# Kernel tuning notes

Hardware: AMD Instinct MI355X
Metric: run time of the kernel (lower is better)

Reference implementation:

```python
import jax, jax.numpy as jnp
import numpy as np

NUM_HEADS = 16
HEAD_DIM = 128
WINDOW = 512
ROPE_BASE = 10000.0


def _rope_cos_sin(seq_len):
    inv_freq = 1.0 / (ROPE_BASE ** (jnp.arange(0, HEAD_DIM, 2, dtype=jnp.float32) / HEAD_DIM))
    freqs = jnp.arange(seq_len, dtype=jnp.float32)[:, None] * inv_freq[None, :]  # (s, d/2)
    return jnp.cos(freqs), jnp.sin(freqs)


def _apply_rotary(x, cos, sin):
    # x: (b, h, s, d); cos/sin: (s, d/2). Interleaved pairs as in the torch impl.
    x1, x2 = x[..., ::2], x[..., 1::2]
    c = cos[None, None]
    s = sin[None, None]
    r1 = x1 * c - x2 * s
    r2 = x1 * s + x2 * c
    return jnp.stack([r1, r2], axis=-1).reshape(x.shape)


def setup_inputs() -> dict:
    key = jax.random.key(0)
    ks = jax.random.split(key, 5)
    dim = NUM_HEADS * HEAD_DIM
    x = jax.random.normal(ks[0], (1, 4096, dim), dtype=jnp.float32)
    std = 0.02
    Wq = jax.random.normal(ks[1], (dim, dim), dtype=jnp.float32) * std
    Wk = jax.random.normal(ks[2], (dim, dim), dtype=jnp.float32) * std
    Wv = jax.random.normal(ks[3], (dim, dim), dtype=jnp.float32) * std
    Wo = jax.random.normal(ks[4], (dim, dim), dtype=jnp.float32) * std
    return {"x": x, "Wq": Wq, "Wk": Wk, "Wv": Wv, "Wo": Wo}


def reference(x, Wq, Wk, Wv, Wo):
    b, s, dim = x.shape
    scale = HEAD_DIM ** -0.5

    def split_heads(t):
        return t.reshape(b, s, NUM_HEADS, HEAD_DIM).transpose(0, 2, 1, 3)  # b h s d

    q = split_heads(x @ Wq.T)
    k = split_heads(x @ Wk.T)
    v = split_heads(x @ Wv.T)

    cos, sin = _rope_cos_sin(s)
    q = _apply_rotary(q, cos, sin)
    k = _apply_rotary(k, cos, sin)

    scores = jnp.einsum('bhqd,bhkd->bhqk', q, k) * scale  # (b, h, s, s)
    pos = jnp.arange(s)
    i, j = pos[:, None], pos[None, :]
    mask = (j <= i) & (i - j < WINDOW)  # sliding-window causal
    scores = jnp.where(mask[None, None], scores, -jnp.inf)
    attn = jax.nn.softmax(scores, axis=-1)

    out = jnp.einsum('bhqk,bhkd->bhqd', attn, v)
    out = out.transpose(0, 2, 1, 3).reshape(b, s, dim)
    return out @ Wo.T
```

## Files before the change

kernel.cpp:

```cpp
#include <hip/hip_runtime.h>
#include <hip/hip_bf16.h>
#include <math.h>

#define DIM 2048
#define NH 16
#define HD 128
#define WIN 512

typedef __hip_bfloat16 bf16;
using frag8 = __attribute__((ext_vector_type(8))) short;
using facc4 = __attribute__((ext_vector_type(4))) float;

__device__ inline float toF(const bf16 v) { return __bfloat162float(v); }
template <typename T> __device__ inline T fromF(float v);
template <> __device__ inline float fromF<float>(float v) { return v; }
template <> __device__ inline bf16 fromF<bf16>(float v) { return __float2bfloat16(v); }

__device__ inline unsigned bfb(float x) {
    unsigned u = __float_as_uint(x);
    u += 0x7fffu + ((u >> 16) & 1u);
    return u >> 16;
}

__device__ inline uint4 pack8(const float* p) {
    const float4 v0 = *(const float4*)p;
    const float4 v1 = *(const float4*)(p + 4);
    uint4 r;
    r.x = bfb(v0.x) | (bfb(v0.y) << 16);
    r.y = bfb(v0.z) | (bfb(v0.w) << 16);
    r.z = bfb(v1.x) | (bfb(v1.y) << 16);
    r.w = bfb(v1.z) | (bfb(v1.w) << 16);
    return r;
}

__global__ __launch_bounds__(256) void cvt_f32_bf16(const float* __restrict__ src,
                                                    bf16* __restrict__ dst, int n8) {
    const int i = blockIdx.x * 256 + threadIdx.x;
    if (i < n8) ((uint4*)dst)[i] = pack8(src + (size_t)i * 8);
}

#define W8LOG 19
__global__ __launch_bounds__(256) void cvt4_f32_bf16(const float* __restrict__ s0,
                                                     const float* __restrict__ s1,
                                                     const float* __restrict__ s2,
                                                     const float* __restrict__ s3,
                                                     bf16* __restrict__ dst) {
    const int i = blockIdx.x * 256 + threadIdx.x;
    const int seg = i >> W8LOG;
    const int off = i & ((1 << W8LOG) - 1);
    const float* s = (seg == 0) ? s0 : (seg == 1) ? s1 : (seg == 2) ? s2 : s3;
    ((uint4*)dst)[i] = pack8(s + (size_t)off * 8);
}

__device__ inline void gload_lds16(const bf16* g, short* l) {
    __builtin_amdgcn_global_load_lds(
        (const __attribute__((address_space(1))) unsigned int*)g,
        (__attribute__((address_space(3))) unsigned int*)l, 16, 0, 0);
}


#define WAIT_LGKM0()                                             \
    do {                                                         \
        asm volatile("s_waitcnt lgkmcnt(0)" ::: "memory");       \
        __builtin_amdgcn_sched_barrier(0);                       \
    } while (0)

#define READ_A(BUF, MI)                                                          \
    do {                                                                         \
        _Pragma("unroll") for (int ii = 0; ii < 4; ++ii)                         \
        _Pragma("unroll") for (int kk = 0; kk < 2; ++kk) {                       \
            const int row_ = wm * 128 + (MI) * 64 + ii * 16 + mr;                \
            const int slot_ = ((kk << 2) + q) ^ (row_ & 7);                      \
            a[ii][kk] = *(const frag8*)&lds[BUF][0][row_][slot_ << 3];           \
        }                                                                        \
    } while (0)

#define READ_B(BUF, NI)                                                          \
    do {                                                                         \
        _Pragma("unroll") for (int jj = 0; jj < 2; ++jj)                         \
        _Pragma("unroll") for (int kk = 0; kk < 2; ++kk) {                       \
            const int row_ = wn * 64 + (NI) * 32 + jj * 16 + mr;                 \
            const int slot_ = ((kk << 2) + q) ^ (row_ & 7);                      \
            b[NI][jj][kk] = *(const frag8*)&lds[BUF][1][row_][slot_ << 3];       \
        }                                                                        \
    } while (0)

#define MFMA_QUAD(MI, NI)                                                        \
    do {                                                                         \
        __builtin_amdgcn_s_setprio(1);                                           \
        _Pragma("unroll") for (int ii = 0; ii < 4; ++ii)                         \
        _Pragma("unroll") for (int jj = 0; jj < 2; ++jj)                         \
        _Pragma("unroll") for (int kk = 0; kk < 2; ++kk)                         \
            acc[(MI) * 4 + ii][(NI) * 2 + jj] =                                  \
                __builtin_amdgcn_mfma_f32_16x16x32_bf16(                         \
                    a[ii][kk], b[NI][jj][kk], acc[(MI) * 4 + ii][(NI) * 2 + jj], \
                    0, 0, 0);                                                    \
        __builtin_amdgcn_s_setprio(0);                                           \
    } while (0)

template <typename TC, bool SPLIT>
__global__ __launch_bounds__(512, 2) void gemm256_8ph(const bf16* __restrict__ A,
                                                      const bf16* __restrict__ B,
                                                      TC* __restrict__ C,
                                                      bf16* __restrict__ Qp,
                                                      bf16* __restrict__ Kp,
                                                      bf16* __restrict__ Vp,
                                                      int M, int N, int K) {
    __shared__ __align__(16) short lds[2][2][256][64];
    const int tid = threadIdx.x;
    const int lane = tid & 63;
    const int w = tid >> 6;

    const int gx = gridDim.x;
    const int nwg = gx * (int)gridDim.y;
    const int lin0 = (int)blockIdx.y * gx + (int)blockIdx.x;
    const int lin = ((nwg & 7) == 0) ? (lin0 & 7) * (nwg >> 3) + (lin0 >> 3) : lin0;
    const int n0 = (lin % gx) * 256;
    const int m0 = (lin / gx) * 256;

    const int wm = w >> 2, wn = w & 3;
    const int q = lane >> 4, mr = lane & 15;
    const int sl = lane & 7, rlo = lane >> 3;
    const int rbA = wm * 128 + wn * 16;
    const int rbB = (w >> 1) * 64 + (w & 1) * 16;

    const int nt = K >> 6;
    const int nIter = nt >> 1;

    facc4 acc[8][4];
#pragma unroll
    for (int i = 0; i < 8; ++i)
#pragma unroll
        for (int j = 0; j < 4; ++j)
#pragma unroll
            for (int r = 0; r < 4; ++r) acc[i][j][r] = 0.f;

    frag8 a[4][2], b[2][2][2];

    auto stage = [&](const bf16* __restrict__ G, int grb, int mat, int buf, int ub, int t) {
        const int kt = t < nt ? t : nt - 1;
        const int k0 = kt << 6;
#pragma unroll
        for (int u = 0; u < 2; ++u) {
            const int row0 = ub + u * 8;
            const int row = row0 + rlo;
            gload_lds16(G + (size_t)(grb + row) * K + k0 + ((sl ^ rlo) << 3),
                        (short*)&lds[buf][mat][row0][0]);
        }
    };

    stage(A, m0, 0, 0, rbA, 0);
    stage(A, m0, 0, 0, rbA + 64, 0);
    stage(B, n0, 1, 0, rbB, 0);
    stage(B, n0, 1, 0, rbB + 32, 0);
    stage(A, m0, 0, 1, rbA, 1);
    stage(B, n0, 1, 1, rbB, 1);
    stage(B, n0, 1, 1, rbB + 32, 1);
    asm volatile("s_waitcnt vmcnt(6)" ::: "memory");
    __builtin_amdgcn_s_barrier();

    for (int it = 0; it < nIter; ++it) {
        const int t2 = 2 * it + 2;
        READ_A(0, 0);
        READ_B(0, 0);
        stage(A, m0, 0, 1, rbA + 64, 2 * it + 1);
        __builtin_amdgcn_s_barrier();
        WAIT_LGKM0();
        MFMA_QUAD(0, 0);
        __builtin_amdgcn_s_barrier();
        READ_B(0, 1);
        stage(A, m0, 0, 0, rbA, t2);
        __builtin_amdgcn_s_barrier();
        WAIT_LGKM0();
        MFMA_QUAD(0, 1);
        __builtin_amdgcn_s_barrier();
        READ_A(0, 1);
        stage(B, n0, 1, 0, rbB, t2);
        __builtin_amdgcn_s_barrier();
        WAIT_LGKM0();
        MFMA_QUAD(1, 0);
        __builtin_amdgcn_s_barrier();
        stage(B, n0, 1, 0, rbB + 32, t2);
        __builtin_amdgcn_s_barrier();
        __builtin_amdgcn_sched_barrier(0);
        MFMA_QUAD(1, 1);
        asm volatile("s_waitcnt vmcnt(6)" ::: "memory");
        __builtin_amdgcn_s_barrier();
        READ_A(1, 0);
        READ_B(1, 0);
        stage(A, m0, 0, 0, rbA + 64, t2);
        __builtin_amdgcn_s_barrier();
        WAIT_LGKM0();
        MFMA_QUAD(0, 0);
        __builtin_amdgcn_s_barrier();
        READ_B(1, 1);
        stage(A, m0, 0, 1, rbA, t2 + 1);
        __builtin_amdgcn_s_barrier();
        WAIT_LGKM0();
        MFMA_QUAD(0, 1);
        __builtin_amdgcn_s_barrier();
        READ_A(1, 1);
        stage(B, n0, 1, 1, rbB, t2 + 1);
        __builtin_amdgcn_s_barrier();
        WAIT_LGKM0();
        MFMA_QUAD(1, 0);
        __builtin_amdgcn_s_barrier();
        stage(B, n0, 1, 1, rbB + 32, t2 + 1);
        __builtin_amdgcn_s_barrier();
        __builtin_amdgcn_sched_barrier(0);
        MFMA_QUAD(1, 1);
        asm volatile("s_waitcnt vmcnt(6)" ::: "memory");
        __builtin_amdgcn_s_barrier();
    }

    if (SPLIT) {
        if (n0 < 2 * DIM) {
            bf16* dst = (n0 < DIM) ? Qp : Kp;
            const int nb = n0 % DIM;
            const int row0 = m0 + wm * 128 + q * 4;
#pragma unroll
            for (int jn = 0; jn < 4; ++jn) {
                const int col = nb + wn * 64 + jn * 16 + mr;
                const int f = (col & 127) >> 1;
                const float inv = __expf(-0.14391157f * (float)f);
                const float sgn = (col & 1) ? 1.f : -1.f;
                float cb_, sb_, c1, s1, c16, s16;
                sincosf((float)row0 * inv, &sb_, &cb_);
                sincosf(inv, &s1, &c1);
                sincosf(16.f * inv, &s16, &c16);
#pragma unroll
                for (int im = 0; im < 8; ++im) {
                    float c = cb_, s = sb_;
#pragma unroll
                    for (int r = 0; r < 4; ++r) {
                        const float v = acc[im][jn][r];
                        const float p = __shfl_xor(v, 1, 64);
                        dst[(size_t)(row0 + im * 16 + r) * DIM + col] =
                            fromF<bf16>(v * c + sgn * p * s);
                        const float cn = c * c1 - s * s1;
                        const float sn = s * c1 + c * s1;
                        c = cn; s = sn;
                    }
                    const float cbn = cb_ * c16 - sb_ * s16;
                    const float sbn = sb_ * c16 + cb_ * s16;
                    cb_ = cbn; sb_ = sbn;
                }
            }
        } else {
            asm volatile("s_waitcnt vmcnt(0)" ::: "memory");
            __builtin_amdgcn_s_barrier();
            short* sc = (short*)lds;
            const int cb = n0 - 2 * DIM;
            const int colR = tid >> 2;
#pragma unroll
            for (int half = 0; half < 2; ++half) {
                if (half) __builtin_amdgcn_s_barrier();
                if ((wn >> 1) == half) {
#pragma unroll
                    for (int im = 0; im < 8; ++im) {
                        const int s = wm * 128 + im * 16 + q * 4;
#pragma unroll
                        for (int jn = 0; jn < 4; ++jn) {
                            const int cl = (wn & 1) * 64 + jn * 16 + mr;
                            uint2 pk;
                            pk.x = bfb(acc[im][jn][0]) | (bfb(acc[im][jn][1]) << 16);
                            pk.y = bfb(acc[im][jn][2]) | (bfb(acc[im][jn][3]) << 16);
                            *(uint2*)&sc[cl * 264 + s] = pk;
                        }
                    }
                }
                __builtin_amdgcn_s_barrier();
#pragma unroll
                for (int rr = 0; rr < 8; ++rr) {
                    const int s0 = (tid & 3) * 8 + rr * 32;
                    const uint4 v = *(const uint4*)&sc[colR * 264 + s0];
                    *(uint4*)(Vp + (size_t)(cb + half * 128 + colR) * M + m0 + s0) = v;
                }
            }
        }
    } else {
#pragma unroll
        for (int im = 0; im < 8; ++im)
#pragma unroll
            for (int jn = 0; jn < 4; ++jn) {
                const int col = n0 + wn * 64 + jn * 16 + mr;
#pragma unroll
                for (int r = 0; r < 4; ++r) {
                    const int row = m0 + wm * 128 + im * 16 + q * 4 + r;
                    C[(size_t)row * N + col] = fromF<TC>(acc[im][jn][r]);
                }
            }
    }
}

template <typename TC>
__global__ __launch_bounds__(256) void gemm_bt_async(const bf16* __restrict__ A,
                                                     const bf16* __restrict__ B,
                                                     TC* __restrict__ C,
                                                     int M, int N, int K) {
    __shared__ short As[128 * 32];
    __shared__ short Bs[128 * 32];
    const int tid = threadIdx.x;
    const int lane = tid & 63;
    const int w = tid >> 6;
    const int m0 = blockIdx.y * 128;
    const int n0 = blockIdx.x * 128;
    const int wm = (w >> 1) * 64;
    const int wn = (w & 1) * 64;
    const int q = lane >> 4;
    const int mr = lane & 15;

    facc4 acc[4][4];
#pragma unroll
    for (int i = 0; i < 4; ++i)
#pragma unroll
        for (int j = 0; j < 4; ++j)
#pragma unroll
            for (int r = 0; r < 4; ++r) acc[i][j][r] = 0.f;

    for (int k0 = 0; k0 < K; k0 += 32) {
        __syncthreads();
#pragma unroll
        for (int u = 0; u < 2; ++u) {
            const int c = w * 128 + u * 64 + lane;
            const int row = c >> 2, col = (c & 3) * 8;
            gload_lds16(A + (size_t)(m0 + row) * K + k0 + col, As + (w * 128 + u * 64) * 8);
            gload_lds16(B + (size_t)(n0 + row) * K + k0 + col, Bs + (w * 128 + u * 64) * 8);
        }
        __syncthreads();

        frag8 af[4], bfr[4];
#pragma unroll
        for (int i = 0; i < 4; ++i)
            af[i] = *(const frag8*)&As[(wm + 16 * i + mr) * 32 + q * 8];
#pragma unroll
        for (int j = 0; j < 4; ++j)
            bfr[j] = *(const frag8*)&Bs[(wn + 16 * j + mr) * 32 + q * 8];
#pragma unroll
        for (int i = 0; i < 4; ++i)
#pragma unroll
            for (int j = 0; j < 4; ++j)
                acc[i][j] = __builtin_amdgcn_mfma_f32_16x16x32_bf16(af[i], bfr[j], acc[i][j], 0, 0, 0);
    }

#pragma unroll
    for (int i = 0; i < 4; ++i)
#pragma unroll
        for (int j = 0; j < 4; ++j) {
            const int col = n0 + wn + 16 * j + mr;
#pragma unroll
            for (int r = 0; r < 4; ++r) {
                const int row = m0 + wm + 16 * i + q * 4 + r;
                C[(size_t)row * N + col] = fromF<TC>(acc[i][j][r]);
            }
        }
}

__global__ __launch_bounds__(256, 3) void flash_swa(const bf16* __restrict__ Q,
                                                    const bf16* __restrict__ K,
                                                    const bf16* __restrict__ Vt,
                                                    bf16* __restrict__ O, int S) {
    __shared__ __align__(16) char lds[53248];
    short* Qs = (short*)lds;
    short* Ps = (short*)lds;
    short* Ks = (short*)(lds + 17408);
    short* VtL = (short*)(lds + 34816);

    const int tid = threadIdx.x;
    const int lane = tid & 63;
    const int w = tid >> 6;
    const int q = lane >> 4;
    const int mr = lane & 15;
    const int i0 = blockIdx.x * 64;
    const int h = blockIdx.y;
    const float scale = 0.08838834764831845f;

#pragma unroll
    for (int u = 0; u < 4; ++u) {
        const int c = tid + 256 * u;
        const int row = c >> 4, col = (c & 15) * 8;
        *(uint4*)&Qs[row * 136 + col] =
            *(const uint4*)(Q + (size_t)(i0 + row) * DIM + h * HD + col);
    }
    __syncthreads();
    frag8 qf[4];
#pragma unroll
    for (int kk = 0; kk < 4; ++kk)
        qf[kk] = *(const frag8*)&Qs[(w * 16 + mr) * 136 + kk * 32 + q * 8];

    float mrow[4], lrow[4];
    facc4 oacc[8];
#pragma unroll
    for (int r = 0; r < 4; ++r) { mrow[r] = -1e30f; lrow[r] = 0.f; }
#pragma unroll
    for (int dt = 0; dt < 8; ++dt)
#pragma unroll
        for (int r = 0; r < 4; ++r) oacc[dt][r] = 0.f;

    const bf16* vtg = Vt + (size_t)h * HD * S;

    const int t0 = (i0 >= WIN) ? 0 : (WIN - i0) / 64;
    for (int t = t0; t < 9; ++t) {
        const int jb = i0 - WIN + t * 64;
        __syncthreads();

#pragma unroll
        for (int u = 0; u < 4; ++u) {
            const int c = tid + 256 * u;
            const int row = c >> 4, col = (c & 15) * 8;
            *(uint4*)&Ks[row * 136 + col] =
                *(const uint4*)(K + (size_t)(jb + row) * DIM + h * HD + col);
        }
#pragma unroll
        for (int u = 0; u < 4; ++u) {
            const int c = tid + 256 * u;
            const int d = c >> 3, k0c = (c & 7) * 8;
            *(uint4*)&VtL[d * 72 + k0c] = *(const uint4*)(vtg + (size_t)d * S + jb + k0c);
        }
        __syncthreads();

        facc4 sacc[4];
#pragma unroll
        for (int nt = 0; nt < 4; ++nt) {
#pragma unroll
            for (int r = 0; r < 4; ++r) sacc[nt][r] = 0.f;
#pragma unroll
            for (int kk = 0; kk < 4; ++kk) {
                const frag8 kfr = *(const frag8*)&Ks[(nt * 16 + mr) * 136 + kk * 32 + q * 8];
                sacc[nt] = __builtin_amdgcn_mfma_f32_16x16x32_bf16(qf[kk], kfr, sacc[nt], 0, 0, 0);
            }
        }

        float sv[4][4];
        float rmax[4] = {-1e30f, -1e30f, -1e30f, -1e30f};
#pragma unroll
        for (int nt = 0; nt < 4; ++nt) {
            const int j = jb + nt * 16 + mr;
#pragma unroll
            for (int r = 0; r < 4; ++r) {
                const int i = i0 + w * 16 + q * 4 + r;
                const bool valid = (j <= i) && (i - j < WIN);
                sv[nt][r] = valid ? sacc[nt][r] * scale : -1e30f;
                rmax[r] = fmaxf(rmax[r], sv[nt][r]);
            }
        }
#pragma unroll
        for (int msk = 1; msk <= 8; msk <<= 1)
#pragma unroll
            for (int r = 0; r < 4; ++r)
                rmax[r] = fmaxf(rmax[r], __shfl_xor(rmax[r], msk, 64));

        float alpha[4], rsum[4];
#pragma unroll
        for (int r = 0; r < 4; ++r) {
            const float mn = fmaxf(mrow[r], rmax[r]);
            alpha[r] = __expf(mrow[r] - mn);
            mrow[r] = mn;
            rsum[r] = 0.f;
        }
#pragma unroll
        for (int nt = 0; nt < 4; ++nt)
#pragma unroll
            for (int r = 0; r < 4; ++r) {
                const float pv = (sv[nt][r] > -1e29f) ? __expf(sv[nt][r] - mrow[r]) : 0.f;
                rsum[r] += pv;
                Ps[(w * 16 + q * 4 + r) * 72 + nt * 16 + mr] = (short)bfb(pv);
            }
#pragma unroll
        for (int msk = 1; msk <= 8; msk <<= 1)
#pragma unroll
            for (int r = 0; r < 4; ++r)
                rsum[r] += __shfl_xor(rsum[r], msk, 64);
#pragma unroll
        for (int r = 0; r < 4; ++r) lrow[r] = lrow[r] * alpha[r] + rsum[r];
#pragma unroll
        for (int dt = 0; dt < 8; ++dt)
#pragma unroll
            for (int r = 0; r < 4; ++r) oacc[dt][r] *= alpha[r];

        __syncthreads();

#pragma unroll
        for (int ks = 0; ks < 2; ++ks) {
            const frag8 pf = *(const frag8*)&Ps[(w * 16 + mr) * 72 + ks * 32 + q * 8];
#pragma unroll
            for (int dt = 0; dt < 8; ++dt) {
                const frag8 vf = *(const frag8*)&VtL[(dt * 16 + mr) * 72 + ks * 32 + q * 8];
                oacc[dt] = __builtin_amdgcn_mfma_f32_16x16x32_bf16(pf, vf, oacc[dt], 0, 0, 0);
            }
        }
    }

    float inv[4];
#pragma unroll
    for (int r = 0; r < 4; ++r) inv[r] = 1.0f / lrow[r];
#pragma unroll
    for (int dt = 0; dt < 8; ++dt)
#pragma unroll
        for (int r = 0; r < 4; ++r) {
            const int row = i0 + w * 16 + q * 4 + r;
            O[(size_t)row * DIM + h * HD + dt * 16 + mr] = fromF<bf16>(oacc[dt][r] * inv[r]);
        }
}

extern "C" void kernel_launch(void* const* d_in, const int* in_sizes, int n_in,
                              void* d_out, int out_size, void* d_ws, size_t ws_size,
                              hipStream_t stream) {
    const float* x  = (const float*)d_in[0];
    const float* Wq = (const float*)d_in[1];
    const float* Wk = (const float*)d_in[2];
    const float* Wv = (const float*)d_in[3];
    const float* Wo = (const float*)d_in[4];
    float* out = (float*)d_out;

    const int S = in_sizes[0] / DIM;
    const size_t elems = (size_t)S * DIM;
    const size_t wsz = (size_t)DIM * DIM;

    bf16* Q    = (bf16*)d_ws;
    bf16* K    = Q + elems;
    bf16* V    = K + elems;
    bf16* Aat  = V + elems;
    bf16* xb   = Aat + elems;
    bf16* Wcat = xb + elems;
    bf16* Wob  = Wcat + 3 * wsz;

    cvt_f32_bf16<<<(int)(elems / 8 / 256), 256, 0, stream>>>(x, xb, (int)(elems / 8));
    cvt4_f32_bf16<<<(int)(4 * wsz / 8 / 256), 256, 0, stream>>>(Wq, Wk, Wv, Wo, Wcat);

    gemm256_8ph<bf16, true><<<dim3(3 * DIM / 256, S / 256), 512, 0, stream>>>(
        xb, Wcat, (bf16*)nullptr, Q, K, V, S, 3 * DIM, DIM);

    flash_swa<<<dim3(S / 64, NH), 256, 0, stream>>>(Q, K, V, Aat, S);

    gemm_bt_async<float><<<dim3(DIM / 128, S / 128), 256, 0, stream>>>(
        Aat, Wob, out, S, DIM, DIM);
}
```

Baseline: 379.1 us.

## Prefetch next K/V tile into registers and raise MFMA wave priority

The attention loop now loads the next 64-key K and V^T tiles from global memory into registers while the current tile is being computed. At the top of each iteration those registers are written into shared memory, so global load latency overlaps with the QK and PV MFMA work. The MFMA sections are wrapped in s_setprio, and the barrier before the PV stage is dropped, since each wave reads only the Ps rows it wrote itself. This costs extra VGPRs for the staging buffers, which may lower occupancy.

```diff
diff --git a/kernel.cpp b/kernel.cpp
--- a/kernel.cpp
+++ b/kernel.cpp
@@ -399,37 +399,57 @@
 
     const bf16* vtg = Vt + (size_t)h * HD * S;
 
+    const bf16* kbase = K + (size_t)(tid >> 4) * DIM + h * HD + (tid & 15) * 8;
+    const bf16* vbase = vtg + (size_t)(tid >> 3) * S + (tid & 7) * 8;
+    short* kdst = &Ks[(tid >> 4) * 136 + (tid & 15) * 8];
+    short* vdst = &VtL[(tid >> 3) * 72 + (tid & 7) * 8];
+
     const int t0 = (i0 >= WIN) ? 0 : (WIN - i0) / 64;
+    uint4 kst[4], vst[4];
+    {
+        const int jb = i0 - WIN + t0 * 64;
+#pragma unroll
+        for (int u = 0; u < 4; ++u) {
+            kst[u] = *(const uint4*)(kbase + (size_t)(jb + 16 * u) * DIM);
+            vst[u] = *(const uint4*)(vbase + (size_t)(32 * u) * S + jb);
+        }
+    }
+
     for (int t = t0; t < 9; ++t) {
         const int jb = i0 - WIN + t * 64;
         __syncthreads();
-
 #pragma unroll
         for (int u = 0; u < 4; ++u) {
-            const int c = tid + 256 * u;
-            const int row = c >> 4, col = (c & 15) * 8;
-            *(uint4*)&Ks[row * 136 + col] =
-                *(const uint4*)(K + (size_t)(jb + row) * DIM + h * HD + col);
-        }
-#pragma unroll
-        for (int u = 0; u < 4; ++u) {
-            const int c = tid + 256 * u;
-            const int d = c >> 3, k0c = (c & 7) * 8;
-            *(uint4*)&VtL[d * 72 + k0c] = *(const uint4*)(vtg + (size_t)d * S + jb + k0c);
+            *(uint4*)(kdst + u * 16 * 136) = kst[u];
+            *(uint4*)(vdst + u * 32 * 72) = vst[u];
         }
         __syncthreads();
 
+        if (t < 8) {
+            const int jbn = jb + 64;
+#pragma unroll
+            for (int u = 0; u < 4; ++u) {
+                kst[u] = *(const uint4*)(kbase + (size_t)(jbn + 16 * u) * DIM);
+                vst[u] = *(const uint4*)(vbase + (size_t)(32 * u) * S + jbn);
+            }
+        }
+
         facc4 sacc[4];
 #pragma unroll
         for (int nt = 0; nt < 4; ++nt) {
 #pragma unroll
             for (int r = 0; r < 4; ++r) sacc[nt][r] = 0.f;
+        }
+        __builtin_amdgcn_s_setprio(1);
+#pragma unroll
+        for (int nt = 0; nt < 4; ++nt) {
 #pragma unroll
             for (int kk = 0; kk < 4; ++kk) {
                 const frag8 kfr = *(const frag8*)&Ks[(nt * 16 + mr) * 136 + kk * 32 + q * 8];
                 sacc[nt] = __builtin_amdgcn_mfma_f32_16x16x32_bf16(qf[kk], kfr, sacc[nt], 0, 0, 0);
             }
         }
+        __builtin_amdgcn_s_setprio(0);
 
         float sv[4][4];
         float rmax[4] = {-1e30f, -1e30f, -1e30f, -1e30f};
@@ -478,8 +498,7 @@
 #pragma unroll
             for (int r = 0; r < 4; ++r) oacc[dt][r] *= alpha[r];
 
-        __syncthreads();
-
+        __builtin_amdgcn_s_setprio(1);
 #pragma unroll
         for (int ks = 0; ks < 2; ++ks) {
             const frag8 pf = *(const frag8*)&Ps[(w * 16 + mr) * 72 + ks * 32 + q * 8];
@@ -489,6 +508,7 @@
                 oacc[dt] = __builtin_amdgcn_mfma_f32_16x16x32_bf16(pf, vf, oacc[dt], 0, 0, 0);
             }
         }
+        __builtin_amdgcn_s_setprio(0);
     }
 
     float inv[4];
```

Result: slower. 439.4 us (+15.9%).

## Double-buffer K/V tiles in flash attention with async global-to-LDS loads

Applied to the files above, without the earlier changes.

Rewrites the sliding-window attention kernel's K/V staging into a two-deep pipeline. Tiles move straight from global memory into LDS with direct loads, and the next tile is fetched while the current one is computed. The kernel also reads Q fragments directly from global memory, uses an XOR-swizzled LDS layout instead of padding, and remaps block indices to spread query tiles across blocks. It adds s_setprio around the MFMA sections and guards with explicit vmcnt waits and barriers. The larger LDS footprint lowers the occupancy bound from 3 to 2 blocks per CU, and the manual wait counts and clamped tail prefetch risk correctness or pipeline stalls.

```diff
diff --git a/kernel.cpp b/kernel.cpp
--- a/kernel.cpp
+++ b/kernel.cpp
@@ -356,37 +356,56 @@
         }
 }
 
-__global__ __launch_bounds__(256, 3) void flash_swa(const bf16* __restrict__ Q,
+__global__ __launch_bounds__(256, 2) void flash_swa(const bf16* __restrict__ Q,
                                                     const bf16* __restrict__ K,
                                                     const bf16* __restrict__ Vt,
                                                     bf16* __restrict__ O, int S) {
-    __shared__ __align__(16) char lds[53248];
-    short* Qs = (short*)lds;
-    short* Ps = (short*)lds;
-    short* Ks = (short*)(lds + 17408);
-    short* VtL = (short*)(lds + 34816);
+    __shared__ __align__(16) char lds[74752];
+    short* Ksl = (short*)lds;
+    short* Vtl = (short*)(lds + 32768);
+    short* Ps  = (short*)(lds + 65536);
 
     const int tid = threadIdx.x;
     const int lane = tid & 63;
     const int w = tid >> 6;
     const int q = lane >> 4;
     const int mr = lane & 15;
-    const int i0 = blockIdx.x * 64;
+    const int bx = blockIdx.x;
+    const int i0 = (((bx & 7) << 3) | (bx >> 3)) * 64;
     const int h = blockIdx.y;
     const float scale = 0.08838834764831845f;
-
+    const int sw = mr & 7;
+
+    frag8 qf[4];
+    const bf16* qptr = Q + (size_t)(i0 + w * 16 + mr) * DIM + h * HD + q * 8;
+#pragma unroll
+    for (int kk = 0; kk < 4; ++kk) qf[kk] = *(const frag8*)(qptr + kk * 32);
+
+    const bf16* vtg = Vt + (size_t)h * HD * S;
+
+    int koff[4], voff[4];
 #pragma unroll
     for (int u = 0; u < 4; ++u) {
-        const int c = tid + 256 * u;
-        const int row = c >> 4, col = (c & 15) * 8;
-        *(uint4*)&Qs[row * 136 + col] =
-            *(const uint4*)(Q + (size_t)(i0 + row) * DIM + h * HD + col);
+        const int krow = w * 16 + 4 * u + (lane >> 4);
+        const int kch = (lane & 15) ^ (krow & 7);
+        koff[u] = krow * DIM + h * HD + kch * 8;
+        const int vrow = w * 32 + 8 * u + (lane >> 3);
+        const int vch = (lane & 7) ^ (vrow & 7);
+        voff[u] = vrow * S + vch * 8;
     }
-    __syncthreads();
-    frag8 qf[4];
-#pragma unroll
-    for (int kk = 0; kk < 4; ++kk)
-        qf[kk] = *(const frag8*)&Qs[(w * 16 + mr) * 136 + kk * 32 + q * 8];
+
+    auto issue = [&](int t, int buf) {
+        int jb = i0 - WIN + t * 64;
+        if (jb > S - 64) jb = S - 64;
+        const bf16* kb = K + (size_t)jb * DIM;
+        const bf16* vb = vtg + jb;
+#pragma unroll
+        for (int u = 0; u < 4; ++u)
+            gload_lds16(kb + koff[u], Ksl + buf * 8192 + (w * 16 + 4 * u) * 128);
+#pragma unroll
+        for (int u = 0; u < 4; ++u)
+            gload_lds16(vb + voff[u], Vtl + buf * 8192 + (w * 32 + 8 * u) * 64);
+    };
 
     float mrow[4], lrow[4];
     facc4 oacc[8];
@@ -397,39 +416,33 @@
 #pragma unroll
         for (int r = 0; r < 4; ++r) oacc[dt][r] = 0.f;
 
-    const bf16* vtg = Vt + (size_t)h * HD * S;
-
     const int t0 = (i0 >= WIN) ? 0 : (WIN - i0) / 64;
+    issue(t0, 0);
+    issue(t0 + 1, 1);
+    int p = 0;
+
     for (int t = t0; t < 9; ++t) {
         const int jb = i0 - WIN + t * 64;
-        __syncthreads();
-
-#pragma unroll
-        for (int u = 0; u < 4; ++u) {
-            const int c = tid + 256 * u;
-            const int row = c >> 4, col = (c & 15) * 8;
-            *(uint4*)&Ks[row * 136 + col] =
-                *(const uint4*)(K + (size_t)(jb + row) * DIM + h * HD + col);
-        }
-#pragma unroll
-        for (int u = 0; u < 4; ++u) {
-            const int c = tid + 256 * u;
-            const int d = c >> 3, k0c = (c & 7) * 8;
-            *(uint4*)&VtL[d * 72 + k0c] = *(const uint4*)(vtg + (size_t)d * S + jb + k0c);
-        }
-        __syncthreads();
+        asm volatile("s_waitcnt vmcnt(8)" ::: "memory");
+        __builtin_amdgcn_s_barrier();
+        __builtin_amdgcn_sched_barrier(0);
 
         facc4 sacc[4];
 #pragma unroll
+        for (int nt = 0; nt < 4; ++nt)
+#pragma unroll
+            for (int r = 0; r < 4; ++r) sacc[nt][r] = 0.f;
+        __builtin_amdgcn_s_setprio(1);
+#pragma unroll
         for (int nt = 0; nt < 4; ++nt) {
 #pragma unroll
-            for (int r = 0; r < 4; ++r) sacc[nt][r] = 0.f;
-#pragma unroll
             for (int kk = 0; kk < 4; ++kk) {
-                const frag8 kfr = *(const frag8*)&Ks[(nt * 16 + mr) * 136 + kk * 32 + q * 8];
+                const frag8 kfr = *(const frag8*)&Ksl[p * 8192 + (nt * 16 + mr) * 128 +
+                                                      (((kk * 4 + q) ^ sw) << 3)];
                 sacc[nt] = __builtin_amdgcn_mfma_f32_16x16x32_bf16(qf[kk], kfr, sacc[nt], 0, 0, 0);
             }
         }
+        __builtin_amdgcn_s_setprio(0);
 
         float sv[4][4];
         float rmax[4] = {-1e30f, -1e30f, -1e30f, -1e30f};
@@ -478,18 +491,25 @@
 #pragma unroll
             for (int r = 0; r < 4; ++r) oacc[dt][r] *= alpha[r];
 
-        __syncthreads();
-
+        __builtin_amdgcn_s_setprio(1);
 #pragma unroll
         for (int ks = 0; ks < 2; ++ks) {
             const frag8 pf = *(const frag8*)&Ps[(w * 16 + mr) * 72 + ks * 32 + q * 8];
 #pragma unroll
             for (int dt = 0; dt < 8; ++dt) {
-                const frag8 vf = *(const frag8*)&VtL[(dt * 16 + mr) * 72 + ks * 32 + q * 8];
+                const frag8 vf = *(const frag8*)&Vtl[p * 8192 + (dt * 16 + mr) * 64 +
+                                                     (((ks * 4 + q) ^ sw) << 3)];
                 oacc[dt] = __builtin_amdgcn_mfma_f32_16x16x32_bf16(pf, vf, oacc[dt], 0, 0, 0);
             }
         }
+        __builtin_amdgcn_s_setprio(0);
+
+        __builtin_amdgcn_s_barrier();
+        __builtin_amdgcn_sched_barrier(0);
+        issue(t + 2, p);
+        p ^= 1;
     }
+    asm volatile("s_waitcnt vmcnt(0)" ::: "memory");
 
     float inv[4];
 #pragma unroll
```

Result: no change. 375.5 us (-0.9%).
